# Performance work log

Measured on AMD Instinct MI355X. Metric: run time of the kernel, lower is better.

The kernel has to match this reference:

```python
import math
import jax, jax.numpy as jnp
import numpy as np

IN_DIM = 512
OUT_DIM = 100000
BATCH = 512
S = 64.0
M = 0.5
EPS = 1e-12  # matches F.normalize eps


def setup_inputs() -> dict:
    key = jax.random.key(0)
    kx, kw, ky = jax.random.split(key, 3)
    x = jax.random.normal(kx, (BATCH, IN_DIM), dtype=jnp.float32)
    # nn.init.normal_(weights, std=0.01)
    W = 0.01 * jax.random.normal(kw, (IN_DIM, OUT_DIM), dtype=jnp.float32)
    y = jax.random.randint(ky, (BATCH,), 0, OUT_DIM, dtype=jnp.int64)
    nc = 10
    return {"x": x, "W": W, "y": y, "nc": nc}


def reference(x, W, y, nc):
    # FC: L2-normalize rows of x and columns of W, cosine GEMM, clamp.
    x_norm = x / jnp.maximum(jnp.linalg.norm(x, axis=-1, keepdims=True), EPS)
    w_norm = W / jnp.maximum(jnp.linalg.norm(W, axis=0, keepdims=True), EPS)
    cosine = jnp.clip(jnp.einsum('bi,ic->bc', x_norm, w_norm), -1.0, 1.0)  # [B, C]

    b = jnp.arange(x.shape[0])
    target = cosine[b, y]                      # cosine at ground-truth class, [B]
    theta = jnp.arccos(target)

    # no-grad block: intra scores + hard-negative topk over classes
    intra_scores = jax.lax.stop_gradient(target)
    neg_cosine = jax.lax.stop_gradient(cosine).at[b, y].set(-1.0)
    _, hard_indexes = jax.lax.top_k(neg_cosine, nc)  # [B, nc]

    # angular margin: add m where theta < pi - m, else linear penalty
    mask = theta < (math.pi - M)
    margin_cosine = jnp.where(mask,
                              jnp.cos(theta + M),
                              jnp.cos(theta) - math.sin(math.pi - M) * M)

    logits = S * cosine.at[b, y].set(margin_cosine)
    return logits, intra_scores, hard_indexes
```

## Files before the change

kernel.cpp:

```cpp
#include <hip/hip_runtime.h>

#define IN_DIM 512
#define BATCH  512
#define NCLS   100000
#define NC     10
#define NTILE  782

using half8_t  = __attribute__((ext_vector_type(8))) _Float16;
using floatx4  = __attribute__((ext_vector_type(4))) float;

__global__ __launch_bounds__(256) void k_prep(const float* __restrict__ x,
                                              const int* __restrict__ yraw,
                                              _Float16* __restrict__ xhi,
                                              _Float16* __restrict__ xlo,
                                              float* __restrict__ invx,
                                              int* __restrict__ yflag) {
  int b = blockIdx.x, t = threadIdx.x;
  __shared__ float red[256];
  float v0 = x[b * IN_DIM + t];
  float v1 = x[b * IN_DIM + t + 256];
  red[t] = v0 * v0 + v1 * v1;
  __syncthreads();
  for (int s = 128; s > 0; s >>= 1) {
    if (t < s) red[t] += red[t + s];
    __syncthreads();
  }
  if (t == 0) invx[b] = 1.0f / fmaxf(sqrtf(red[0]), 1e-12f);

  float s0 = v0 * 16.f, s1 = v1 * 16.f;
  _Float16 h0 = (_Float16)s0, h1 = (_Float16)s1;
  xhi[b * IN_DIM + t]       = h0;
  xhi[b * IN_DIM + t + 256] = h1;
  xlo[b * IN_DIM + t]       = (_Float16)(s0 - (float)h0);
  xlo[b * IN_DIM + t + 256] = (_Float16)(s1 - (float)h1);

  if (b == 0 && t == 0) {
    int allz = 1;
    for (int i = 1; i < 512; i += 2) allz &= (yraw[i] == 0);
    *yflag = allz;
  }
}

__global__ __launch_bounds__(256, 2) void k_gemm(const _Float16* __restrict__ xhi,
                                                 const _Float16* __restrict__ xlo,
                                                 const float* __restrict__ W,
                                                 const float* __restrict__ invx,
                                                 const int* __restrict__ yraw,
                                                 const int* __restrict__ yflag,
                                                 float* __restrict__ tilemax,
                                                 float* __restrict__ out) {
  __shared__ half8_t lAhi[512], lAlo[512], lBhi[512], lBlo[512];
  __shared__ float   ssred[512];
  __shared__ float   invwn[128];
  __shared__ int     clsb[128];

  const int t = threadIdx.x;
  const int bid = blockIdx.x;
  const int g2  = (bid & 7) * 391 + (bid >> 3);
  const int ct  = g2 >> 2;
  const int m0  = (g2 & 3) * 128;
  const int c0  = ct * 128;

  const int g    = t >> 6;
  const int lane = t & 63;
  const int cpl  = lane * 2;
  const bool cval = (c0 + cpl) < NCLS;

  const int w  = t >> 6;
  const int ll = t & 63;
  const int wm = ((w >> 1) & 1) * 64;
  const int wn = (w & 1) * 64;
  const int ko = ll >> 4, lm = ll & 15;

  if (t < 128) clsb[t] = (*yflag) ? yraw[2 * (m0 + t)] : yraw[m0 + t];

  floatx4 acc[4][4] = {};
  float ss0 = 0.f, ss1 = 0.f;

  for (int ks = 0; ks < 16; ks++) {
    const int k0 = ks * 32;
#pragma unroll
    for (int h = 0; h < 2; h++) {
      int p  = t + h * 256;
      int pk = p >> 7, pm = p & 127;
      size_t off = (size_t)(m0 + pm) * IN_DIM + (size_t)(k0 + pk * 8);
      lAhi[p] = *(const half8_t*)(xhi + off);
      lAlo[p] = *(const half8_t*)(xlo + off);
    }
    half8_t b0h, b0l, b1h, b1l;
#pragma unroll
    for (int r = 0; r < 8; r++) {
      float w0 = 0.f, w1 = 0.f;
      if (cval) {
        const float2 wv = *(const float2*)(W + (size_t)(k0 + g * 8 + r) * NCLS + (c0 + cpl));
        w0 = wv.x; w1 = wv.y;
      }
      ss0 += w0 * w0;
      ss1 += w1 * w1;
      float sw0 = w0 * 256.f, sw1 = w1 * 256.f;
      _Float16 h0 = (_Float16)sw0, h1 = (_Float16)sw1;
      b0h[r] = h0; b1h[r] = h1;
      b0l[r] = (_Float16)(sw0 - (float)h0);
      b1l[r] = (_Float16)(sw1 - (float)h1);
    }
    {
      int bi0 = g * 128 + (cpl >> 1);
      lBhi[bi0] = b0h; lBhi[bi0 + 64] = b1h;
      lBlo[bi0] = b0l; lBlo[bi0 + 64] = b1l;
    }
    __syncthreads();

    half8_t ah[4], al[4], bh[4], bl[4];
#pragma unroll
    for (int i = 0; i < 4; i++) {
      int am = wm + i * 16 + lm;
      ah[i] = lAhi[ko * 128 + am];
      al[i] = lAlo[ko * 128 + am];
      int cl = wn + i * 16 + lm;
      int bidx = ko * 128 + ((cl & 1) << 6) + (cl >> 1);
      bh[i] = lBhi[bidx];
      bl[i] = lBlo[bidx];
    }
#pragma unroll
    for (int i = 0; i < 4; i++)
#pragma unroll
      for (int j = 0; j < 4; j++) {
        acc[i][j] = __builtin_amdgcn_mfma_f32_16x16x32_f16(ah[i], bh[j], acc[i][j], 0, 0, 0);
        acc[i][j] = __builtin_amdgcn_mfma_f32_16x16x32_f16(ah[i], bl[j], acc[i][j], 0, 0, 0);
        acc[i][j] = __builtin_amdgcn_mfma_f32_16x16x32_f16(al[i], bh[j], acc[i][j], 0, 0, 0);
      }
    __syncthreads();
  }

  ssred[cpl * 4 + g]       = ss0;
  ssred[(cpl + 1) * 4 + g] = ss1;
  __syncthreads();
  if (t < 128) {
    float s = ssred[t * 4] + ssred[t * 4 + 1] + ssred[t * 4 + 2] + ssred[t * 4 + 3];
    invwn[t] = (1.0f / 4096.0f) / fmaxf(sqrtf(s), 1e-12f);
  }
  __syncthreads();

  float rmax[4][4];
#pragma unroll
  for (int i = 0; i < 4; i++)
#pragma unroll
    for (int rr = 0; rr < 4; rr++) rmax[i][rr] = -3.402823466e38f;

#pragma unroll
  for (int i = 0; i < 4; i++) {
#pragma unroll
    for (int rr = 0; rr < 4; rr++) {
      int rl = wm + i * 16 + ko * 4 + rr;
      int rg = m0 + rl;
      float ix = invx[rg];
      int mycls = clsb[rl];
#pragma unroll
      for (int j = 0; j < 4; j++) {
        int cl = wn + j * 16 + lm;
        int cg = c0 + cl;
        if (cg < NCLS) {
          float v = acc[i][j][rr] * ix * invwn[cl];
          v = fminf(fmaxf(v, -1.f), 1.f) * 64.f;
          out[(size_t)rg * NCLS + cg] = v;
          if (cg != mycls) rmax[i][rr] = fmaxf(rmax[i][rr], v);
        }
      }
    }
  }
#pragma unroll
  for (int i = 0; i < 4; i++)
#pragma unroll
    for (int rr = 0; rr < 4; rr++) {
#pragma unroll
      for (int off = 1; off < 16; off <<= 1)
        rmax[i][rr] = fmaxf(rmax[i][rr], __shfl_xor(rmax[i][rr], off));
    }
  if (lm == 0) {
#pragma unroll
    for (int i = 0; i < 4; i++)
#pragma unroll
      for (int rr = 0; rr < 4; rr++)
        ssred[(wm + i * 16 + ko * 4 + rr) * 2 + (w & 1)] = rmax[i][rr];
  }
  __syncthreads();
  if (t < 128)
    tilemax[(size_t)ct * BATCH + m0 + t] = fmaxf(ssred[t * 2], ssred[t * 2 + 1]);
}

__global__ __launch_bounds__(256) void k_fix(const float* __restrict__ x,
                                             const float* __restrict__ W,
                                             const int* __restrict__ yraw,
                                             const int* __restrict__ yflag,
                                             const float* __restrict__ invx,
                                             float* __restrict__ out) {
  int b = blockIdx.x, t = threadIdx.x;
  int cls = (*yflag) ? yraw[2 * b] : yraw[b];
  __shared__ float rd[256], rs[256];
  float dot = 0.f, ssw = 0.f;
#pragma unroll
  for (int h = 0; h < 2; h++) {
    int k   = t + h * 256;
    float xv = x[b * IN_DIM + k];
    float wv = W[(size_t)k * NCLS + cls];
    dot += xv * wv;
    ssw += wv * wv;
  }
  rd[t] = dot; rs[t] = ssw;
  __syncthreads();
  for (int s = 128; s > 0; s >>= 1) {
    if (t < s) { rd[t] += rd[t + s]; rs[t] += rs[t + s]; }
    __syncthreads();
  }
  if (t == 0) {
    float iw  = 1.0f / fmaxf(sqrtf(rs[0]), 1e-12f);
    float tgt = rd[0] * invx[b] * iw;
    tgt = fminf(fmaxf(tgt, -1.f), 1.f);
    out[(size_t)BATCH * NCLS + b] = tgt;
    const float cosM = 0.87758256189037271612f;
    const float sinM = 0.47942553860420300027f;
    float mc;
    if (tgt > -cosM)
      mc = tgt * cosM - sqrtf(fmaxf(1.f - tgt * tgt, 0.f)) * sinM;
    else
      mc = tgt - sinM * 0.5f;
    out[(size_t)b * NCLS + cls] = 64.f * mc;
  }
}

__global__ __launch_bounds__(256) void k_topk(const float* __restrict__ logits,
                                              const float* __restrict__ tmaxArr,
                                              const int* __restrict__ yraw,
                                              const int* __restrict__ yflag,
                                              float* __restrict__ outIdx) {
  const int b = blockIdx.x, t = threadIdx.x;
  const int cls = (*yflag) ? yraw[2 * b] : yraw[b];

  __shared__ float lv[2560];
  __shared__ int   li[2560];
  __shared__ float cv[256];
  __shared__ int   ci[256];
  __shared__ int   cp[256];
  __shared__ int   list[NTILE];
  __shared__ int   cnt;
  __shared__ float stau;

  float vals[10]; int idxs[10];
#pragma unroll
  for (int i = 0; i < 10; i++) { vals[i] = -3.402823466e38f; idxs[i] = 0x7fffffff; }

  for (int T = t; T < NTILE; T += 256) {
    float v = tmaxArr[(size_t)T * BATCH + b];
    if (v > vals[9] || (v == vals[9] && T < idxs[9])) {
      float cv2 = v; int ci2 = T;
#pragma unroll
      for (int p = 0; p < 10; p++) {
        bool better = (cv2 > vals[p]) || (cv2 == vals[p] && ci2 < idxs[p]);
        if (better) {
          float tv = vals[p]; int ti = idxs[p];
          vals[p] = cv2; idxs[p] = ci2;
          cv2 = tv; ci2 = ti;
        }
      }
    }
  }
#pragma unroll
  for (int i = 0; i < 10; i++) { lv[t * 10 + i] = vals[i]; li[t * 10 + i] = idxs[i]; }
  if (t == 0) cnt = 0;
  __syncthreads();

  for (int r = 0; r < NC; r++) {
    float bv = -3.402823466e38f; int bi = 0x7fffffff; int bp = -1;
#pragma unroll
    for (int i = 0; i < 10; i++) {
      int e = t * 10 + i;
      float v = lv[e];
      if (v > bv || (v == bv && li[e] < bi)) { bv = v; bi = li[e]; bp = e; }
    }
    cv[t] = bv; ci[t] = bi; cp[t] = bp;
    __syncthreads();
    for (int s = 128; s > 0; s >>= 1) {
      if (t < s) {
        if (cv[t + s] > cv[t] || (cv[t + s] == cv[t] && ci[t + s] < ci[t])) {
          cv[t] = cv[t + s]; ci[t] = ci[t + s]; cp[t] = cp[t + s];
        }
      }
      __syncthreads();
    }
    if (t == 0) {
      lv[cp[0]] = -3.402823466e38f;
      if (r == NC - 1) stau = cv[0];
    }
    __syncthreads();
  }
  const float tau = stau;

  for (int T = t; T < NTILE; T += 256)
    if (tmaxArr[(size_t)T * BATCH + b] >= tau) { int p = atomicAdd(&cnt, 1); list[p] = T; }
  __syncthreads();
  const int n = cnt;

#pragma unroll
  for (int i = 0; i < 10; i++) { vals[i] = -3.402823466e38f; idxs[i] = 0x7fffffff; }
  const float* row = logits + (size_t)b * NCLS;
  for (int kk = t; kk < n * 128; kk += 256) {
    int T = list[kk >> 7];
    int c = T * 128 + (kk & 127);
    if (c >= NCLS || c == cls) continue;
    float v = row[c];
    if (v > vals[9] || (v == vals[9] && c < idxs[9])) {
      float cv2 = v; int ci2 = c;
#pragma unroll
      for (int p = 0; p < 10; p++) {
        bool better = (cv2 > vals[p]) || (cv2 == vals[p] && ci2 < idxs[p]);
        if (better) {
          float tv = vals[p]; int ti = idxs[p];
          vals[p] = cv2; idxs[p] = ci2;
          cv2 = tv; ci2 = ti;
        }
      }
    }
  }
#pragma unroll
  for (int i = 0; i < 10; i++) { lv[t * 10 + i] = vals[i]; li[t * 10 + i] = idxs[i]; }
  __syncthreads();

  for (int r = 0; r < NC; r++) {
    float bv = -3.402823466e38f; int bi = 0x7fffffff; int bp = -1;
#pragma unroll
    for (int i = 0; i < 10; i++) {
      int e = t * 10 + i;
      float v = lv[e];
      if (v > bv || (v == bv && li[e] < bi)) { bv = v; bi = li[e]; bp = e; }
    }
    cv[t] = bv; ci[t] = bi; cp[t] = bp;
    __syncthreads();
    for (int s = 128; s > 0; s >>= 1) {
      if (t < s) {
        if (cv[t + s] > cv[t] || (cv[t + s] == cv[t] && ci[t + s] < ci[t])) {
          cv[t] = cv[t + s]; ci[t] = ci[t + s]; cp[t] = cp[t + s];
        }
      }
      __syncthreads();
    }
    if (t == 0) {
      outIdx[b * NC + r] = (float)ci[0];
      lv[cp[0]] = -3.402823466e38f;
    }
    __syncthreads();
  }
}

extern "C" void kernel_launch(void* const* d_in, const int* in_sizes, int n_in,
                              void* d_out, int out_size, void* d_ws, size_t ws_size,
                              hipStream_t stream) {
  const float* x = (const float*)d_in[0];
  const float* W = (const float*)d_in[1];
  const int*   y = (const int*)d_in[2];
  float* out = (float*)d_out;
  char*  ws  = (char*)d_ws;

  _Float16* xhi  = (_Float16*)ws;
  _Float16* xlo  = (_Float16*)(ws + (1 << 19));
  float*    invx = (float*)(ws + (1 << 20));
  int*      yfl  = (int*)(ws + (1 << 20) + 4096);
  float*    tmax = (float*)(ws + (1 << 20) + 8192);

  k_prep<<<BATCH, 256, 0, stream>>>(x, y, xhi, xlo, invx, yfl);
  k_gemm<<<dim3(8 * 391), 256, 0, stream>>>(xhi, xlo, W, invx, y, yfl, tmax, out);
  k_fix<<<BATCH, 256, 0, stream>>>(x, W, y, yfl, invx, out);
  k_topk<<<BATCH, 256, 0, stream>>>(out, tmax, y, yfl, out + (size_t)BATCH * NCLS + BATCH);
}
```

Baseline: 636.9 us.

## Pre-split W into transposed fp16 hi/lo buffers once per call before the GEMM

Measured after the change: 695.0 us. +9.1%, slower.

```diff
diff --git a/kernel.cpp b/kernel.cpp
--- a/kernel.cpp
+++ b/kernel.cpp
@@ -3,10 +3,12 @@
 #define IN_DIM 512
 #define BATCH  512
 #define NCLS   100000
+#define NCPAD  100096
 #define NC     10
 #define NTILE  782
 
 using half8_t  = __attribute__((ext_vector_type(8))) _Float16;
+using ushort8  = __attribute__((ext_vector_type(8))) unsigned short;
 using floatx4  = __attribute__((ext_vector_type(4))) float;
 
 __global__ __launch_bounds__(256) void k_prep(const float* __restrict__ x,
@@ -41,16 +43,63 @@
   }
 }
 
-__global__ __launch_bounds__(256, 2) void k_gemm(const _Float16* __restrict__ xhi,
-                                                 const _Float16* __restrict__ xlo,
-                                                 const float* __restrict__ W,
-                                                 const float* __restrict__ invx,
-                                                 const int* __restrict__ yraw,
-                                                 const int* __restrict__ yflag,
-                                                 float* __restrict__ tilemax,
-                                                 float* __restrict__ out) {
-  __shared__ half8_t lAhi[512], lAlo[512], lBhi[512], lBlo[512];
-  __shared__ float   ssred[512];
+__global__ __launch_bounds__(256) void k_wsplit(const float* __restrict__ W,
+                                                unsigned short* __restrict__ WhiT,
+                                                unsigned short* __restrict__ WloT,
+                                                float* __restrict__ invwG) {
+  __shared__ unsigned short sHi[64][72];
+  __shared__ unsigned short sLo[64][72];
+  __shared__ float ssred[256];
+  const int t    = threadIdx.x;
+  const int c0   = blockIdx.x * 64;
+  const int lane = t & 63;
+  const int grp  = t >> 6;
+  const int c    = c0 + lane;
+  float ss = 0.f;
+
+  for (int kb = 0; kb < 8; kb++) {
+#pragma unroll
+    for (int it = 0; it < 16; it++) {
+      int kl = grp * 16 + it;
+      int k  = kb * 64 + kl;
+      float w = (c < NCLS) ? W[(size_t)k * NCLS + c] : 0.f;
+      ss += w * w;
+      float sw = w * 256.f;
+      _Float16 h = (_Float16)sw;
+      _Float16 l = (_Float16)(sw - (float)h);
+      sHi[lane][kl] = __builtin_bit_cast(unsigned short, h);
+      sLo[lane][kl] = __builtin_bit_cast(unsigned short, l);
+    }
+    __syncthreads();
+#pragma unroll
+    for (int q = 0; q < 2; q++) {
+      int v = t + q * 256;
+      int col = v >> 3, s = v & 7;
+      ushort8 hv = *(const ushort8*)&sHi[col][s * 8];
+      ushort8 lv = *(const ushort8*)&sLo[col][s * 8];
+      size_t o = (size_t)(c0 + col) * IN_DIM + kb * 64 + s * 8;
+      *(ushort8*)(WhiT + o) = hv;
+      *(ushort8*)(WloT + o) = lv;
+    }
+    __syncthreads();
+  }
+  ssred[t] = ss;
+  __syncthreads();
+  if (t < 64) {
+    float tot = ssred[t] + ssred[t + 64] + ssred[t + 128] + ssred[t + 192];
+    invwG[c0 + t] = (1.0f / 4096.0f) / fmaxf(sqrtf(tot), 1e-12f);
+  }
+}
+
+__global__ __launch_bounds__(256, 2) void k_gemm_fast(
+    const _Float16* __restrict__ xhi, const _Float16* __restrict__ xlo,
+    const unsigned short* __restrict__ WhiT, const unsigned short* __restrict__ WloT,
+    const float* __restrict__ invx, const float* __restrict__ invwG,
+    const int* __restrict__ yraw, const int* __restrict__ yflag,
+    float* __restrict__ tilemax, float* __restrict__ out) {
+  __shared__ half8_t lAhi[512], lAlo[512];
+  __shared__ ushort8 lBhi[640], lBlo[640];
+  __shared__ float   rred[256];
   __shared__ float   invwn[128];
   __shared__ int     clsb[128];
 
@@ -61,21 +110,19 @@
   const int m0  = (g2 & 3) * 128;
   const int c0  = ct * 128;
 
-  const int g    = t >> 6;
-  const int lane = t & 63;
-  const int cpl  = lane * 2;
-  const bool cval = (c0 + cpl) < NCLS;
-
   const int w  = t >> 6;
   const int ll = t & 63;
   const int wm = ((w >> 1) & 1) * 64;
   const int wn = (w & 1) * 64;
   const int ko = ll >> 4, lm = ll & 15;
 
-  if (t < 128) clsb[t] = (*yflag) ? yraw[2 * (m0 + t)] : yraw[m0 + t];
+  if (t < 128) {
+    int cg = c0 + t;
+    invwn[t] = (cg < NCLS) ? invwG[cg] : 0.f;
+    clsb[t]  = (*yflag) ? yraw[2 * (m0 + t)] : yraw[m0 + t];
+  }
 
   floatx4 acc[4][4] = {};
-  float ss0 = 0.f, ss1 = 0.f;
 
   for (int ks = 0; ks < 16; ks++) {
     const int k0 = ks * 32;
@@ -87,26 +134,13 @@
       lAhi[p] = *(const half8_t*)(xhi + off);
       lAlo[p] = *(const half8_t*)(xlo + off);
     }
-    half8_t b0h, b0l, b1h, b1l;
-#pragma unroll
-    for (int r = 0; r < 8; r++) {
-      float w0 = 0.f, w1 = 0.f;
-      if (cval) {
-        const float2 wv = *(const float2*)(W + (size_t)(k0 + g * 8 + r) * NCLS + (c0 + cpl));
-        w0 = wv.x; w1 = wv.y;
-      }
-      ss0 += w0 * w0;
-      ss1 += w1 * w1;
-      float sw0 = w0 * 256.f, sw1 = w1 * 256.f;
-      _Float16 h0 = (_Float16)sw0, h1 = (_Float16)sw1;
-      b0h[r] = h0; b1h[r] = h1;
-      b0l[r] = (_Float16)(sw0 - (float)h0);
-      b1l[r] = (_Float16)(sw1 - (float)h1);
-    }
-    {
-      int bi0 = g * 128 + (cpl >> 1);
-      lBhi[bi0] = b0h; lBhi[bi0 + 64] = b1h;
-      lBlo[bi0] = b0l; lBlo[bi0 + 64] = b1l;
+#pragma unroll
+    for (int q = 0; q < 2; q++) {
+      int u = t + q * 256;
+      int col = u >> 2, ch = u & 3;
+      size_t boff = (size_t)(c0 + col) * IN_DIM + (size_t)(k0 + ch * 8);
+      lBhi[col * 5 + ch] = *(const ushort8*)(WhiT + boff);
+      lBlo[col * 5 + ch] = *(const ushort8*)(WloT + boff);
     }
     __syncthreads();
 
@@ -117,9 +151,8 @@
       ah[i] = lAhi[ko * 128 + am];
       al[i] = lAlo[ko * 128 + am];
       int cl = wn + i * 16 + lm;
-      int bidx = ko * 128 + ((cl & 1) << 6) + (cl >> 1);
-      bh[i] = lBhi[bidx];
-      bl[i] = lBlo[bidx];
+      bh[i] = __builtin_bit_cast(half8_t, lBhi[cl * 5 + ko]);
+      bl[i] = __builtin_bit_cast(half8_t, lBlo[cl * 5 + ko]);
     }
 #pragma unroll
     for (int i = 0; i < 4; i++)
@@ -131,15 +164,6 @@
       }
     __syncthreads();
   }
-
-  ssred[cpl * 4 + g]       = ss0;
-  ssred[(cpl + 1) * 4 + g] = ss1;
-  __syncthreads();
-  if (t < 128) {
-    float s = ssred[t * 4] + ssred[t * 4 + 1] + ssred[t * 4 + 2] + ssred[t * 4 + 3];
-    invwn[t] = (1.0f / 4096.0f) / fmaxf(sqrtf(s), 1e-12f);
-  }
-  __syncthreads();
 
   float rmax[4][4];
 #pragma unroll
@@ -181,11 +205,177 @@
     for (int i = 0; i < 4; i++)
 #pragma unroll
       for (int rr = 0; rr < 4; rr++)
+        rred[(wm + i * 16 + ko * 4 + rr) * 2 + (w & 1)] = rmax[i][rr];
+  }
+  __syncthreads();
+  if (t < 128)
+    tilemax[(size_t)ct * BATCH + m0 + t] = fmaxf(rred[t * 2], rred[t * 2 + 1]);
+}
+
+__global__ __launch_bounds__(256, 2) void k_gemm_fb(const _Float16* __restrict__ xhi,
+                                                    const _Float16* __restrict__ xlo,
+                                                    const float* __restrict__ W,
+                                                    const float* __restrict__ invx,
+                                                    const int* __restrict__ yraw,
+                                                    const int* __restrict__ yflag,
+                                                    float* __restrict__ tilemax,
+                                                    float* __restrict__ out) {
+  __shared__ half8_t lAhi[512], lAlo[512], lBhi[512], lBlo[512];
+  __shared__ float   ssred[512];
+  __shared__ float   invwn[128];
+  __shared__ int     clsb[128];
+
+  const int t = threadIdx.x;
+  const int bid = blockIdx.x;
+  const int g2  = (bid & 7) * 391 + (bid >> 3);
+  const int ct  = g2 >> 2;
+  const int m0  = (g2 & 3) * 128;
+  const int c0  = ct * 128;
+
+  const int g    = t >> 6;
+  const int lane = t & 63;
+  const int cpl  = lane * 2;
+  const bool cval = (c0 + cpl) < NCLS;
+
+  const int w  = t >> 6;
+  const int ll = t & 63;
+  const int wm = ((w >> 1) & 1) * 64;
+  const int wn = (w & 1) * 64;
+  const int ko = ll >> 4, lm = ll & 15;
+
+  if (t < 128) clsb[t] = (*yflag) ? yraw[2 * (m0 + t)] : yraw[m0 + t];
+
+  floatx4 acc[4][4] = {};
+  float ss0 = 0.f, ss1 = 0.f;
+
+  for (int ks = 0; ks < 16; ks++) {
+    const int k0 = ks * 32;
+#pragma unroll
+    for (int h = 0; h < 2; h++) {
+      int p  = t + h * 256;
+      int pk = p >> 7, pm = p & 127;
+      size_t off = (size_t)(m0 + pm) * IN_DIM + (size_t)(k0 + pk * 8);
+      lAhi[p] = *(const half8_t*)(xhi + off);
+      lAlo[p] = *(const half8_t*)(xlo + off);
+    }
+    half8_t b0h, b0l, b1h, b1l;
+#pragma unroll
+    for (int r = 0; r < 8; r++) {
+      float w0 = 0.f, w1 = 0.f;
+      if (cval) {
+        const float2 wv = *(const float2*)(W + (size_t)(k0 + g * 8 + r) * NCLS + (c0 + cpl));
+        w0 = wv.x; w1 = wv.y;
+      }
+      ss0 += w0 * w0;
+      ss1 += w1 * w1;
+      float sw0 = w0 * 256.f, sw1 = w1 * 256.f;
+      _Float16 h0 = (_Float16)sw0, h1 = (_Float16)sw1;
+      b0h[r] = h0; b1h[r] = h1;
+      b0l[r] = (_Float16)(sw0 - (float)h0);
+      b1l[r] = (_Float16)(sw1 - (float)h1);
+    }
+    {
+      int bi0 = g * 128 + (cpl >> 1);
+      lBhi[bi0] = b0h; lBhi[bi0 + 64] = b1h;
+      lBlo[bi0] = b0l; lBlo[bi0 + 64] = b1l;
+    }
+    __syncthreads();
+
+    half8_t ah[4], al[4], bh[4], bl[4];
+#pragma unroll
+    for (int i = 0; i < 4; i++) {
+      int am = wm + i * 16 + lm;
+      ah[i] = lAhi[ko * 128 + am];
+      al[i] = lAlo[ko * 128 + am];
+      int cl = wn + i * 16 + lm;
+      int bidx = ko * 128 + ((cl & 1) << 6) + (cl >> 1);
+      bh[i] = lBhi[bidx];
+      bl[i] = lBlo[bidx];
+    }
+#pragma unroll
+    for (int i = 0; i < 4; i++)
+#pragma unroll
+      for (int j = 0; j < 4; j++) {
+        acc[i][j] = __builtin_amdgcn_mfma_f32_16x16x32_f16(ah[i], bh[j], acc[i][j], 0, 0, 0);
+        acc[i][j] = __builtin_amdgcn_mfma_f32_16x16x32_f16(ah[i], bl[j], acc[i][j], 0, 0, 0);
+        acc[i][j] = __builtin_amdgcn_mfma_f32_16x16x32_f16(al[i], bh[j], acc[i][j], 0, 0, 0);
+      }
+    __syncthreads();
+  }
+
+  ssred[cpl * 4 + g]       = ss0;
+  ssred[(cpl + 1) * 4 + g] = ss1;
+  __syncthreads();
+  if (t < 128) {
+    float s = ssred[t * 4] + ssred[t * 4 + 1] + ssred[t * 4 + 2] + ssred[t * 4 + 3];
+    invwn[t] = (1.0f / 4096.0f) / fmaxf(sqrtf(s), 1e-12f);
+  }
+  __syncthreads();
+
+  float rmax[4][4];
+#pragma unroll
+  for (int i = 0; i < 4; i++)
+#pragma unroll
+    for (int rr = 0; rr < 4; rr++) rmax[i][rr] = -3.402823466e38f;
+
+#pragma unroll
+  for (int i = 0; i < 4; i++) {
+#pragma unroll
+    for (int rr = 0; rr < 4; rr++) {
+      int rl = wm + i * 16 + ko * 4 + rr;
+      int rg = m0 + rl;
+      float ix = invx[rg];
+      int mycls = clsb[rl];
+#pragma unroll
+      for (int j = 0; j < 4; j++) {
+        int cl = wn + j * 16 + lm;
+        int cg = c0 + cl;
+        if (cg < NCLS) {
+          float v = acc[i][j][rr] * ix * invwn[cl];
+          v = fminf(fmaxf(v, -1.f), 1.f) * 64.f;
+          out[(size_t)rg * NCLS + cg] = v;
+          if (cg != mycls) rmax[i][rr] = fmaxf(rmax[i][rr], v);
+        }
+      }
+    }
+  }
+#pragma unroll
+  for (int i = 0; i < 4; i++)
+#pragma unroll
+    for (int rr = 0; rr < 4; rr++) {
+#pragma unroll
+      for (int off = 1; off < 16; off <<= 1)
+        rmax[i][rr] = fmaxf(rmax[i][rr], __shfl_xor(rmax[i][rr], off));
+    }
+  if (lm == 0) {
+#pragma unroll
+    for (int i = 0; i < 4; i++)
+#pragma unroll
+      for (int rr = 0; rr < 4; rr++)
         ssred[(wm + i * 16 + ko * 4 + rr) * 2 + (w & 1)] = rmax[i][rr];
   }
   __syncthreads();
   if (t < 128)
     tilemax[(size_t)ct * BATCH + m0 + t] = fmaxf(ssred[t * 2], ssred[t * 2 + 1]);
+}
+
+__global__ __launch_bounds__(256) void k_tmt(const float* __restrict__ in,
+                                             float* __restrict__ outT) {
+  __shared__ float tile[32][33];
+  int T0 = blockIdx.x * 32, r0 = blockIdx.y * 32;
+  int tx = threadIdx.x & 31, ty = threadIdx.x >> 5;
+#pragma unroll
+  for (int i = 0; i < 32; i += 8) {
+    int T = T0 + ty + i;
+    if (T < NTILE) tile[ty + i][tx] = in[(size_t)T * BATCH + r0 + tx];
+  }
+  __syncthreads();
+#pragma unroll
+  for (int i = 0; i < 32; i += 8) {
+    int r = r0 + ty + i;
+    int T = T0 + tx;
+    if (T < NTILE) outT[(size_t)r * NTILE + T] = tile[tx][ty + i];
+  }
 }
 
 __global__ __launch_bounds__(256) void k_fix(const float* __restrict__ x,
@@ -229,12 +419,13 @@
 }
 
 __global__ __launch_bounds__(256) void k_topk(const float* __restrict__ logits,
-                                              const float* __restrict__ tmaxArr,
+                                              const float* __restrict__ tmaxT,
                                               const int* __restrict__ yraw,
                                               const int* __restrict__ yflag,
                                               float* __restrict__ outIdx) {
   const int b = blockIdx.x, t = threadIdx.x;
   const int cls = (*yflag) ? yraw[2 * b] : yraw[b];
+  const float* tm = tmaxT + (size_t)b * NTILE;
 
   __shared__ float lv[2560];
   __shared__ int   li[2560];
@@ -250,7 +441,7 @@
   for (int i = 0; i < 10; i++) { vals[i] = -3.402823466e38f; idxs[i] = 0x7fffffff; }
 
   for (int T = t; T < NTILE; T += 256) {
-    float v = tmaxArr[(size_t)T * BATCH + b];
+    float v = tm[T];
     if (v > vals[9] || (v == vals[9] && T < idxs[9])) {
       float cv2 = v; int ci2 = T;
 #pragma unroll
@@ -296,7 +487,7 @@
   const float tau = stau;
 
   for (int T = t; T < NTILE; T += 256)
-    if (tmaxArr[(size_t)T * BATCH + b] >= tau) { int p = atomicAdd(&cnt, 1); list[p] = T; }
+    if (tm[T] >= tau) { int p = atomicAdd(&cnt, 1); list[p] = T; }
   __syncthreads();
   const int n = cnt;
 
@@ -360,14 +551,26 @@
   float* out = (float*)d_out;
   char*  ws  = (char*)d_ws;
 
-  _Float16* xhi  = (_Float16*)ws;
-  _Float16* xlo  = (_Float16*)(ws + (1 << 19));
-  float*    invx = (float*)(ws + (1 << 20));
-  int*      yfl  = (int*)(ws + (1 << 20) + 4096);
-  float*    tmax = (float*)(ws + (1 << 20) + 8192);
+  _Float16*       xhi  = (_Float16*)ws;
+  _Float16*       xlo  = (_Float16*)(ws + (1 << 19));
+  float*          invx = (float*)(ws + (1 << 20));
+  int*            yfl  = (int*)(ws + (1 << 20) + 4096);
+  float*          invw = (float*)(ws + (1 << 20) + 8192);
+  float*          tmax = (float*)(ws + (2 << 20));
+  float*          tmxT = (float*)(ws + (4 << 20));
+  unsigned short* WhiT = (unsigned short*)(ws + ((size_t)8 << 20));
+  unsigned short* WloT = (unsigned short*)(ws + ((size_t)112 << 20));
+  const size_t WS_NEED = ((size_t)112 << 20) + (size_t)NCPAD * IN_DIM * 2;
 
   k_prep<<<BATCH, 256, 0, stream>>>(x, y, xhi, xlo, invx, yfl);
-  k_gemm<<<dim3(8 * 391), 256, 0, stream>>>(xhi, xlo, W, invx, y, yfl, tmax, out);
+  if (ws_size >= WS_NEED) {
+    k_wsplit<<<NCPAD / 64, 256, 0, stream>>>(W, WhiT, WloT, invw);
+    k_gemm_fast<<<dim3(8 * 391), 256, 0, stream>>>(xhi, xlo, WhiT, WloT, invx, invw,
+                                                   y, yfl, tmax, out);
+  } else {
+    k_gemm_fb<<<dim3(8 * 391), 256, 0, stream>>>(xhi, xlo, W, invx, y, yfl, tmax, out);
+  }
+  k_tmt<<<dim3(25, 16), 256, 0, stream>>>(tmax, tmxT);
   k_fix<<<BATCH, 256, 0, stream>>>(x, W, y, yfl, invx, out);
-  k_topk<<<BATCH, 256, 0, stream>>>(out, tmax, y, yfl, out + (size_t)BATCH * NCLS + BATCH);
-}
+  k_topk<<<BATCH, 256, 0, stream>>>(out, tmxT, y, yfl, out + (size_t)BATCH * NCLS + BATCH);
+}
```
